# Kernel optimization log

Measured on AMD Instinct MI355X. Metric: run time of the kernel, lower is better.

## Reference

```python
import jax, jax.numpy as jnp
import numpy as np

NUM_HEADS = 16
SRC_FACTS = 4


def setup_inputs() -> dict:
    key = jax.random.key(0)
    k1, k2, k3, k4, k5 = jax.random.split(key, 5)
    B, S, H, Dh = 16, 512, NUM_HEADS, 64  # B = batch(4) * src_facts(4)
    D = H * Dh  # d_model = 1024
    pre_q = jax.random.normal(k1, (B, S, H, Dh), dtype=jnp.float32)
    pre_v = jax.random.normal(k2, (B, S, H, Dh), dtype=jnp.float32)
    pre_k = jax.random.normal(k3, (B, S, H, Dh), dtype=jnp.float32)
    attn_mask = jax.random.randint(k4, (B, S, S), 0, 2).astype(jnp.int32)
    output_weights = jax.random.normal(k5, (D, D), dtype=jnp.float32) / np.float32(np.sqrt(D))
    return {
        "pre_q": pre_q,
        "pre_v": pre_v,
        "pre_k": pre_k,
        "attn_mask": attn_mask,
        "output_weights": output_weights,
        "out_seq_len": 512,
        "d_model": 1024,
    }


def reference(pre_q, pre_v, pre_k, attn_mask, output_weights, out_seq_len, d_model):
    B, Sq, H, Dh = pre_q.shape
    # Original: K.sqrt(cast(d_model) // num_heads) -> sqrt(head_dim)
    scale = jnp.sqrt(jnp.float32(float(d_model) // H))
    mask = attn_mask.astype(jnp.float32)[:, None]  # (B, 1, q, k) broadcast over heads
    # scores: (B, H, q, k)
    scores = jnp.einsum("bqhd,bkhd->bhqk", pre_q, pre_k) / scale
    # multiplicative pre-mask + additive -1e9 on masked slots
    scores = scores * mask + (1.0 - mask) * jnp.float32(-1e9)
    # softmax then multiplicative post-mask
    attn = jax.nn.softmax(scores, axis=-1) * mask
    heads = jnp.einsum("bhqk,bkhd->bqhd", attn, pre_v)  # (B, q, H, Dh)
    out = heads.reshape(B, Sq, H * Dh) @ output_weights  # (B, q, d_model)
    return out.reshape(-1, SRC_FACTS, out_seq_len, d_model)
```

## Files before the change

kernel.cpp:

```cpp
#include <hip/hip_runtime.h>
#include <hip/hip_bf16.h>


typedef __bf16 bf16;
typedef bf16 bf16x8 __attribute__((ext_vector_type(8)));
typedef float floatx4 __attribute__((ext_vector_type(4)));
typedef unsigned short ushort8 __attribute__((ext_vector_type(8)));
typedef unsigned long long u64;

#define MFMA16(A, B, C) __builtin_amdgcn_mfma_f32_16x16x32_bf16((A), (B), (C), 0, 0, 0)

namespace {
constexpr int S   = 512;
constexpr int H   = 16;
constexpr int Dh  = 64;
constexpr int D   = 1024;
constexpr int LDT = 72;
constexpr size_t QN = (size_t)16 * S * H * Dh;
constexpr size_t WN = (size_t)D * D;
}

__global__ __launch_bounds__(256)
void prep_kernel(const float* __restrict__ Kf, const float* __restrict__ Vf,
                 const float* __restrict__ Wf, const int* __restrict__ Mg,
                 bf16* __restrict__ Kc, bf16* __restrict__ Vt,
                 bf16* __restrict__ Wt, u64* __restrict__ MB)
{
    __shared__ bf16 Ts[64 * LDT];
    const int blk = blockIdx.x, tid = threadIdx.x;

    if (blk < 4096) {
        const int i = blk * 256 + tid;
        const float* fs = Kf + (size_t)i * 8;
        bf16x8 v;
#pragma unroll
        for (int j = 0; j < 8; ++j) v[j] = (bf16)fs[j];
        *(bf16x8*)(Kc + (size_t)i * 8) = v;
    } else if (blk < 6144) {
        const int bk2 = blk - 4096;
        const int bh  = bk2 >> 3, st = bk2 & 7;
        const int b   = bh >> 4, h = bh & 15;
        const int r   = tid >> 2, c = (tid & 3) * 16;
        const float* src = Vf + ((size_t)((b * S + st * 64 + r) * H + h)) * Dh + c;
#pragma unroll
        for (int i = 0; i < 16; ++i)
            Ts[(c + i) * LDT + r] = (bf16)src[i];
        __syncthreads();
        bf16* dst = Vt + ((size_t)bh * 64 + r) * S + st * 64 + c;
        *(ushort8*)dst       = *(const ushort8*)&Ts[r * LDT + c];
        *(ushort8*)(dst + 8) = *(const ushort8*)&Ts[r * LDT + c + 8];
    } else if (blk < 6400) {
        const int bk2 = blk - 6144;
        const int nb  = bk2 & 15, kb = bk2 >> 4;
        const int r   = tid >> 2, c = (tid & 3) * 16;
        const float* src = Wf + (size_t)(kb * 64 + r) * D + nb * 64 + c;
#pragma unroll
        for (int i = 0; i < 16; ++i)
            Ts[(c + i) * LDT + r] = (bf16)src[i];
        __syncthreads();
        bf16* dst = Wt + (size_t)(nb * 64 + r) * D + kb * 64 + c;
        *(ushort8*)dst       = *(const ushort8*)&Ts[r * LDT + c];
        *(ushort8*)(dst + 8) = *(const ushort8*)&Ts[r * LDT + c + 8];
    } else {
        const int bk2  = blk - 6400;
        const int lane = tid & 63;
        const int idx4 = bk2 * 4 + (tid >> 6);
        const int row  = idx4 >> 1;
        const int half = idx4 & 1;
#pragma unroll
        for (int r = 0; r < 4; ++r) {
            int mv = Mg[(size_t)row * 512 + half * 256 + r * 64 + lane];
            u64 bm = __ballot(mv != 0);
            if (lane == 0) MB[(size_t)row * 8 + half * 4 + r] = bm;
        }
    }
}

__global__ __launch_bounds__(256)
void attn_kernel(const float* __restrict__ Qg, const bf16* __restrict__ Kc,
                 const bf16* __restrict__ Vtg, const u64* __restrict__ MB,
                 bf16* __restrict__ heads)
{
    __shared__ bf16 smem[(128 + 64 + 64) * LDT];
    bf16* Qs = smem;
    bf16* Ps = smem;
    bf16* Ks = smem + 128 * LDT;
    bf16* Vt = smem + 192 * LDT;

    const int tid  = threadIdx.x;
    const int lane = tid & 63;
    const int wave = tid >> 6;
    const int l15  = lane & 15;
    const int quad = lane >> 4;

    const int blk = blockIdx.x;
    const int h   = blk & 15;
    const int qt  = (blk >> 4) & 3;
    const int b   = blk >> 6;
    const int qbase = qt * 128;

    {
        const int pr = tid >> 1, pc = (tid & 1) * 32;
        const float* src = Qg + ((size_t)((b * S + qbase + pr) * H + h)) * Dh + pc;
#pragma unroll
        for (int ch = 0; ch < 4; ++ch) {
            bf16x8 v;
#pragma unroll
            for (int i = 0; i < 8; ++i) v[i] = (bf16)(src[ch * 8 + i] * 0.125f);
            *(bf16x8*)&Qs[pr * LDT + pc + ch * 8] = v;
        }
    }
    __syncthreads();
    bf16x8 aq[2][2];
#pragma unroll
    for (int mt = 0; mt < 2; ++mt)
#pragma unroll
        for (int hf = 0; hf < 2; ++hf)
            aq[mt][hf] = *(const bf16x8*)&Qs[(wave * 32 + mt * 16 + l15) * LDT + hf * 32 + quad * 8];

    float rsum[2][4] = {{0.f}};
    floatx4 O[2][4];
#pragma unroll
    for (int mt = 0; mt < 2; ++mt)
#pragma unroll
        for (int nt = 0; nt < 4; ++nt) O[mt][nt] = floatx4{0.f, 0.f, 0.f, 0.f};

    const int qw = qbase + wave * 32;
    const u64* mb_base = MB + ((size_t)b * S + qw) * 8;
    const bf16* vplane = Vtg + (size_t)(b * 16 + h) * 64 * S;

    const int sr = tid >> 2, sc_ = (tid & 3) * 16;

    for (int kt = 0; kt < 8; ++kt) {
        const int kb = kt * 64;
        const bf16* ksrc = Kc + ((size_t)((b * S + kb + sr) * H + h)) * Dh + sc_;
        const bf16* vsrc = vplane + (size_t)sr * S + kb + sc_;
        ushort8 k0 = *(const ushort8*)ksrc;
        ushort8 k1 = *(const ushort8*)(ksrc + 8);
        ushort8 v0 = *(const ushort8*)vsrc;
        ushort8 v1 = *(const ushort8*)(vsrc + 8);

        __syncthreads();
        *(ushort8*)&Ks[sr * LDT + sc_]     = k0;
        *(ushort8*)&Ks[sr * LDT + sc_ + 8] = k1;
        *(ushort8*)&Vt[sr * LDT + sc_]     = v0;
        *(ushort8*)&Vt[sr * LDT + sc_ + 8] = v1;
        __syncthreads();

        floatx4 sc4[2][4];
#pragma unroll
        for (int nt = 0; nt < 4; ++nt) {
            bf16x8 bk0 = *(const bf16x8*)&Ks[(nt * 16 + l15) * LDT + quad * 8];
            bf16x8 bk1 = *(const bf16x8*)&Ks[(nt * 16 + l15) * LDT + quad * 8 + 32];
#pragma unroll
            for (int mt = 0; mt < 2; ++mt) {
                floatx4 acc = floatx4{0.f, 0.f, 0.f, 0.f};
                acc = MFMA16(aq[mt][0], bk0, acc);
                acc = MFMA16(aq[mt][1], bk1, acc);
                sc4[mt][nt] = acc;
            }
        }

#pragma unroll
        for (int mt = 0; mt < 2; ++mt) {
#pragma unroll
            for (int reg = 0; reg < 4; ++reg) {
                const int row = mt * 16 + quad * 4 + reg;
                u64 m64 = mb_base[(size_t)row * 8 + kt];
                u64 t   = m64 >> l15;
#pragma unroll
                for (int nt = 0; nt < 4; ++nt) {
                    unsigned bit = (unsigned)(t >> (nt * 16)) & 1u;
                    float e = __expf(sc4[mt][nt][reg]);
                    float p = bit ? e : 0.f;
                    rsum[mt][reg] += p;
                    Ps[(wave * 32 + row) * LDT + nt * 16 + l15] = (bf16)p;
                }
            }
        }

#pragma unroll
        for (int nt = 0; nt < 4; ++nt) {
            bf16x8 bv0 = *(const bf16x8*)&Vt[(nt * 16 + l15) * LDT + quad * 8];
            bf16x8 bv1 = *(const bf16x8*)&Vt[(nt * 16 + l15) * LDT + quad * 8 + 32];
#pragma unroll
            for (int mt = 0; mt < 2; ++mt) {
                bf16x8 ap0 = *(const bf16x8*)&Ps[(wave * 32 + mt * 16 + l15) * LDT + quad * 8];
                bf16x8 ap1 = *(const bf16x8*)&Ps[(wave * 32 + mt * 16 + l15) * LDT + quad * 8 + 32];
                O[mt][nt] = MFMA16(ap0, bv0, O[mt][nt]);
                O[mt][nt] = MFMA16(ap1, bv1, O[mt][nt]);
            }
        }
    }

#pragma unroll
    for (int off = 1; off < 16; off <<= 1)
#pragma unroll
        for (int mt = 0; mt < 2; ++mt)
#pragma unroll
            for (int reg = 0; reg < 4; ++reg)
                rsum[mt][reg] += __shfl_xor(rsum[mt][reg], off, 64);

#pragma unroll
    for (int mt = 0; mt < 2; ++mt) {
        float inv[4];
#pragma unroll
        for (int reg = 0; reg < 4; ++reg)
            inv[reg] = (rsum[mt][reg] > 0.f) ? (1.f / rsum[mt][reg]) : 0.f;
#pragma unroll
        for (int nt = 0; nt < 4; ++nt) {
#pragma unroll
            for (int reg = 0; reg < 4; ++reg) {
                const int q = qw + mt * 16 + quad * 4 + reg;
                const int d = nt * 16 + l15;
                heads[((size_t)((b * S + q) * H + h)) * Dh + d] = (bf16)(O[mt][nt][reg] * inv[reg]);
            }
        }
    }
}

__global__ __launch_bounds__(256)
void proj_kernel(const bf16* __restrict__ A, const bf16* __restrict__ Wt,
                 float* __restrict__ out)
{
    __shared__ bf16 As[128 * LDT];
    __shared__ bf16 Ws[128 * LDT];

    const int tid  = threadIdx.x;
    const int lane = tid & 63;
    const int wave = tid >> 6;
    const int l15  = lane & 15;
    const int quad = lane >> 4;

    const int nb = blockIdx.x & 7;
    const int mb = blockIdx.x >> 3;
    const int mbase = mb * 128, nbase = nb * 128;
    const int wm = (wave & 1) * 64, wn = (wave >> 1) * 64;

    const int pr = tid >> 1, pc = (tid & 1) * 32;

    floatx4 O[4][4];
#pragma unroll
    for (int mt = 0; mt < 4; ++mt)
#pragma unroll
        for (int nt = 0; nt < 4; ++nt) O[mt][nt] = floatx4{0.f, 0.f, 0.f, 0.f};

    for (int kt = 0; kt < 16; ++kt) {
        const int kb = kt * 64;
        const bf16* asrc = A  + (size_t)(mbase + pr) * D + kb + pc;
        const bf16* wsrc = Wt + (size_t)(nbase + pr) * D + kb + pc;
        ushort8 a0 = *(const ushort8*)asrc;
        ushort8 a1 = *(const ushort8*)(asrc + 8);
        ushort8 a2 = *(const ushort8*)(asrc + 16);
        ushort8 a3 = *(const ushort8*)(asrc + 24);
        ushort8 w0 = *(const ushort8*)wsrc;
        ushort8 w1 = *(const ushort8*)(wsrc + 8);
        ushort8 w2 = *(const ushort8*)(wsrc + 16);
        ushort8 w3 = *(const ushort8*)(wsrc + 24);

        __syncthreads();
        *(ushort8*)&As[pr * LDT + pc]      = a0;
        *(ushort8*)&As[pr * LDT + pc + 8]  = a1;
        *(ushort8*)&As[pr * LDT + pc + 16] = a2;
        *(ushort8*)&As[pr * LDT + pc + 24] = a3;
        *(ushort8*)&Ws[pr * LDT + pc]      = w0;
        *(ushort8*)&Ws[pr * LDT + pc + 8]  = w1;
        *(ushort8*)&Ws[pr * LDT + pc + 16] = w2;
        *(ushort8*)&Ws[pr * LDT + pc + 24] = w3;
        __syncthreads();

        bf16x8 fa[4][2];
#pragma unroll
        for (int mt = 0; mt < 4; ++mt) {
            fa[mt][0] = *(const bf16x8*)&As[(wm + mt * 16 + l15) * LDT + quad * 8];
            fa[mt][1] = *(const bf16x8*)&As[(wm + mt * 16 + l15) * LDT + quad * 8 + 32];
        }
#pragma unroll
        for (int nt = 0; nt < 4; ++nt) {
            bf16x8 fb0 = *(const bf16x8*)&Ws[(wn + nt * 16 + l15) * LDT + quad * 8];
            bf16x8 fb1 = *(const bf16x8*)&Ws[(wn + nt * 16 + l15) * LDT + quad * 8 + 32];
#pragma unroll
            for (int mt = 0; mt < 4; ++mt) {
                O[mt][nt] = MFMA16(fa[mt][0], fb0, O[mt][nt]);
                O[mt][nt] = MFMA16(fa[mt][1], fb1, O[mt][nt]);
            }
        }
    }

#pragma unroll
    for (int mt = 0; mt < 4; ++mt) {
#pragma unroll
        for (int nt = 0; nt < 4; ++nt) {
#pragma unroll
            for (int reg = 0; reg < 4; ++reg) {
                const int m = mbase + wm + mt * 16 + quad * 4 + reg;
                const int n = nbase + wn + nt * 16 + l15;
                out[(size_t)m * D + n] = O[mt][nt][reg];
            }
        }
    }
}

extern "C" void kernel_launch(void* const* d_in, const int* in_sizes, int n_in,
                              void* d_out, int out_size, void* d_ws, size_t ws_size,
                              hipStream_t stream)
{
    const float* pre_q = (const float*)d_in[0];
    const float* pre_v = (const float*)d_in[1];
    const float* pre_k = (const float*)d_in[2];
    const int*   mask  = (const int*)d_in[3];
    const float* Wg    = (const float*)d_in[4];
    float* out = (float*)d_out;

    bf16* Kc    = (bf16*)d_ws;
    bf16* Vt    = Kc + QN;
    bf16* Wt    = Vt + QN;
    bf16* heads = Wt + WN;
    u64*  MB    = (u64*)(heads + QN);

    prep_kernel<<<10496, 256, 0, stream>>>(pre_k, pre_v, Wg, mask, Kc, Vt, Wt, MB);
    attn_kernel<<<1024, 256, 0, stream>>>(pre_q, Kc, Vt, MB, heads);
    proj_kernel<<<512, 256, 0, stream>>>(heads, Wt, out);
}
```

Measured before the change: 225.9 us.

## Compute transposed scores in registers to skip the P shared-memory round trip

The attention kernel now computes S^T = K·Q^T, with K rows loaded in a permuted order so that the MFMA output registers line up directly with the B-operand layout for the P·V MFMA. This removes the Q and P shared-memory staging and the per-element P stores and reloads. Each wave now handles 16 query rows instead of 32, so the grid doubles and launch bounds request 4 blocks per SM. The trade-off is that every K/V tile is loaded twice as often across blocks, and the mask word is read once per tile per row.

New measurement: 217.1 us. -3.9%, faster.

```diff
diff --git a/kernel.cpp b/kernel.cpp
--- a/kernel.cpp
+++ b/kernel.cpp
@@ -4,11 +4,12 @@
 
 typedef __bf16 bf16;
 typedef bf16 bf16x8 __attribute__((ext_vector_type(8)));
+typedef bf16 bf16x4 __attribute__((ext_vector_type(4)));
 typedef float floatx4 __attribute__((ext_vector_type(4)));
 typedef unsigned short ushort8 __attribute__((ext_vector_type(8)));
 typedef unsigned long long u64;
 
-#define MFMA16(A, B, C) __builtin_amdgcn_mfma_f32_16x16x32_bf16((A), (B), (C), 0, 0, 0)
+#define MFMA32(A, B, C) __builtin_amdgcn_mfma_f32_16x16x32_bf16((A), (B), (C), 0, 0, 0)
 
 namespace {
 constexpr int S   = 512;
@@ -76,16 +77,13 @@
     }
 }
 
-__global__ __launch_bounds__(256)
+__global__ __launch_bounds__(256, 4)
 void attn_kernel(const float* __restrict__ Qg, const bf16* __restrict__ Kc,
                  const bf16* __restrict__ Vtg, const u64* __restrict__ MB,
                  bf16* __restrict__ heads)
 {
-    __shared__ bf16 smem[(128 + 64 + 64) * LDT];
-    bf16* Qs = smem;
-    bf16* Ps = smem;
-    bf16* Ks = smem + 128 * LDT;
-    bf16* Vt = smem + 192 * LDT;
+    __shared__ bf16 Ks[64 * LDT];
+    __shared__ bf16 Vt[64 * LDT];
 
     const int tid  = threadIdx.x;
     const int lane = tid & 63;
@@ -95,50 +93,47 @@
 
     const int blk = blockIdx.x;
     const int h   = blk & 15;
-    const int qt  = (blk >> 4) & 3;
-    const int b   = blk >> 6;
-    const int qbase = qt * 128;
-
+    const int qt  = (blk >> 4) & 7;
+    const int b   = blk >> 7;
+    const int qw  = qt * 64 + wave * 16;
+
+    bf16x8 aq0, aq1;
     {
-        const int pr = tid >> 1, pc = (tid & 1) * 32;
-        const float* src = Qg + ((size_t)((b * S + qbase + pr) * H + h)) * Dh + pc;
-#pragma unroll
-        for (int ch = 0; ch < 4; ++ch) {
-            bf16x8 v;
-#pragma unroll
-            for (int i = 0; i < 8; ++i) v[i] = (bf16)(src[ch * 8 + i] * 0.125f);
-            *(bf16x8*)&Qs[pr * LDT + pc + ch * 8] = v;
-        }
-    }
-    __syncthreads();
-    bf16x8 aq[2][2];
-#pragma unroll
-    for (int mt = 0; mt < 2; ++mt)
-#pragma unroll
-        for (int hf = 0; hf < 2; ++hf)
-            aq[mt][hf] = *(const bf16x8*)&Qs[(wave * 32 + mt * 16 + l15) * LDT + hf * 32 + quad * 8];
-
-    float rsum[2][4] = {{0.f}};
-    floatx4 O[2][4];
-#pragma unroll
-    for (int mt = 0; mt < 2; ++mt)
-#pragma unroll
-        for (int nt = 0; nt < 4; ++nt) O[mt][nt] = floatx4{0.f, 0.f, 0.f, 0.f};
-
-    const int qw = qbase + wave * 32;
-    const u64* mb_base = MB + ((size_t)b * S + qw) * 8;
+        const float* qb = Qg + ((size_t)((b * S + qw + l15) * H + h)) * Dh + quad * 8;
+        floatx4 f0 = *(const floatx4*)qb;
+        floatx4 f1 = *(const floatx4*)(qb + 4);
+        floatx4 f2 = *(const floatx4*)(qb + 32);
+        floatx4 f3 = *(const floatx4*)(qb + 36);
+#pragma unroll
+        for (int j = 0; j < 4; ++j) {
+            aq0[j]     = (bf16)(f0[j] * 0.125f);
+            aq0[j + 4] = (bf16)(f1[j] * 0.125f);
+            aq1[j]     = (bf16)(f2[j] * 0.125f);
+            aq1[j + 4] = (bf16)(f3[j] * 0.125f);
+        }
+    }
+
+    float rsum = 0.f;
+    floatx4 O[4];
+#pragma unroll
+    for (int i = 0; i < 4; ++i) O[i] = floatx4{0.f, 0.f, 0.f, 0.f};
+
+    const u64* mbrow = MB + ((size_t)b * S + qw + l15) * 8;
     const bf16* vplane = Vtg + (size_t)(b * 16 + h) * 64 * S;
 
     const int sr = tid >> 2, sc_ = (tid & 3) * 16;
+    const int kperm = ((sr >> 5) << 5) | (((sr & 15) >> 2) << 3)
+                    | (((sr >> 4) & 1) << 2) | (sr & 3);
 
     for (int kt = 0; kt < 8; ++kt) {
         const int kb = kt * 64;
-        const bf16* ksrc = Kc + ((size_t)((b * S + kb + sr) * H + h)) * Dh + sc_;
+        const bf16* ksrc = Kc + ((size_t)((b * S + kb + kperm) * H + h)) * Dh + sc_;
         const bf16* vsrc = vplane + (size_t)sr * S + kb + sc_;
         ushort8 k0 = *(const ushort8*)ksrc;
         ushort8 k1 = *(const ushort8*)(ksrc + 8);
         ushort8 v0 = *(const ushort8*)vsrc;
         ushort8 v1 = *(const ushort8*)(vsrc + 8);
+        u64 m64 = mbrow[kt];
 
         __syncthreads();
         *(ushort8*)&Ks[sr * LDT + sc_]     = k0;
@@ -147,75 +142,47 @@
         *(ushort8*)&Vt[sr * LDT + sc_ + 8] = v1;
         __syncthreads();
 
-        floatx4 sc4[2][4];
-#pragma unroll
-        for (int nt = 0; nt < 4; ++nt) {
-            bf16x8 bk0 = *(const bf16x8*)&Ks[(nt * 16 + l15) * LDT + quad * 8];
-            bf16x8 bk1 = *(const bf16x8*)&Ks[(nt * 16 + l15) * LDT + quad * 8 + 32];
-#pragma unroll
-            for (int mt = 0; mt < 2; ++mt) {
-                floatx4 acc = floatx4{0.f, 0.f, 0.f, 0.f};
-                acc = MFMA16(aq[mt][0], bk0, acc);
-                acc = MFMA16(aq[mt][1], bk1, acc);
-                sc4[mt][nt] = acc;
-            }
-        }
-
-#pragma unroll
-        for (int mt = 0; mt < 2; ++mt) {
+        bf16x8 pB[2];
+#pragma unroll
+        for (int mt = 0; mt < 4; ++mt) {
+            bf16x8 ak0 = *(const bf16x8*)&Ks[(mt * 16 + l15) * LDT + quad * 8];
+            bf16x8 ak1 = *(const bf16x8*)&Ks[(mt * 16 + l15) * LDT + quad * 8 + 32];
+            floatx4 acc = floatx4{0.f, 0.f, 0.f, 0.f};
+            acc = MFMA32(ak0, aq0, acc);
+            acc = MFMA32(ak1, aq1, acc);
+            const int block = mt >> 1, tile = mt & 1;
+            const int kbase = block * 32 + quad * 8 + tile * 4;
 #pragma unroll
             for (int reg = 0; reg < 4; ++reg) {
-                const int row = mt * 16 + quad * 4 + reg;
-                u64 m64 = mb_base[(size_t)row * 8 + kt];
-                u64 t   = m64 >> l15;
-#pragma unroll
-                for (int nt = 0; nt < 4; ++nt) {
-                    unsigned bit = (unsigned)(t >> (nt * 16)) & 1u;
-                    float e = __expf(sc4[mt][nt][reg]);
-                    float p = bit ? e : 0.f;
-                    rsum[mt][reg] += p;
-                    Ps[(wave * 32 + row) * LDT + nt * 16 + l15] = (bf16)p;
-                }
-            }
-        }
-
-#pragma unroll
-        for (int nt = 0; nt < 4; ++nt) {
-            bf16x8 bv0 = *(const bf16x8*)&Vt[(nt * 16 + l15) * LDT + quad * 8];
-            bf16x8 bv1 = *(const bf16x8*)&Vt[(nt * 16 + l15) * LDT + quad * 8 + 32];
-#pragma unroll
-            for (int mt = 0; mt < 2; ++mt) {
-                bf16x8 ap0 = *(const bf16x8*)&Ps[(wave * 32 + mt * 16 + l15) * LDT + quad * 8];
-                bf16x8 ap1 = *(const bf16x8*)&Ps[(wave * 32 + mt * 16 + l15) * LDT + quad * 8 + 32];
-                O[mt][nt] = MFMA16(ap0, bv0, O[mt][nt]);
-                O[mt][nt] = MFMA16(ap1, bv1, O[mt][nt]);
-            }
-        }
-    }
-
-#pragma unroll
-    for (int off = 1; off < 16; off <<= 1)
-#pragma unroll
-        for (int mt = 0; mt < 2; ++mt)
-#pragma unroll
-            for (int reg = 0; reg < 4; ++reg)
-                rsum[mt][reg] += __shfl_xor(rsum[mt][reg], off, 64);
-
-#pragma unroll
-    for (int mt = 0; mt < 2; ++mt) {
-        float inv[4];
-#pragma unroll
-        for (int reg = 0; reg < 4; ++reg)
-            inv[reg] = (rsum[mt][reg] > 0.f) ? (1.f / rsum[mt][reg]) : 0.f;
-#pragma unroll
-        for (int nt = 0; nt < 4; ++nt) {
-#pragma unroll
-            for (int reg = 0; reg < 4; ++reg) {
-                const int q = qw + mt * 16 + quad * 4 + reg;
-                const int d = nt * 16 + l15;
-                heads[((size_t)((b * S + q) * H + h)) * Dh + d] = (bf16)(O[mt][nt][reg] * inv[reg]);
-            }
-        }
+                unsigned bit = (unsigned)(m64 >> (kbase + reg)) & 1u;
+                float e = __expf(acc[reg]);
+                float p = bit ? e : 0.f;
+                rsum += p;
+                pB[block][tile * 4 + reg] = (bf16)p;
+            }
+        }
+
+#pragma unroll
+        for (int block = 0; block < 2; ++block) {
+#pragma unroll
+            for (int mt = 0; mt < 4; ++mt) {
+                bf16x8 av = *(const bf16x8*)&Vt[(mt * 16 + l15) * LDT + block * 32 + quad * 8];
+                O[mt] = MFMA32(av, pB[block], O[mt]);
+            }
+        }
+    }
+
+    rsum += __shfl_xor(rsum, 16, 64);
+    rsum += __shfl_xor(rsum, 32, 64);
+    const float inv = (rsum > 0.f) ? (1.f / rsum) : 0.f;
+
+    bf16* hrow = heads + ((size_t)((b * S + qw + l15) * H + h)) * Dh;
+#pragma unroll
+    for (int mt = 0; mt < 4; ++mt) {
+        bf16x4 h4;
+#pragma unroll
+        for (int reg = 0; reg < 4; ++reg) h4[reg] = (bf16)(O[mt][reg] * inv);
+        *(bf16x4*)&hrow[mt * 16 + quad * 4] = h4;
     }
 }
 
@@ -281,8 +248,8 @@
             bf16x8 fb1 = *(const bf16x8*)&Ws[(wn + nt * 16 + l15) * LDT + quad * 8 + 32];
 #pragma unroll
             for (int mt = 0; mt < 4; ++mt) {
-                O[mt][nt] = MFMA16(fa[mt][0], fb0, O[mt][nt]);
-                O[mt][nt] = MFMA16(fa[mt][1], fb1, O[mt][nt]);
+                O[mt][nt] = MFMA32(fa[mt][0], fb0, O[mt][nt]);
+                O[mt][nt] = MFMA32(fa[mt][1], fb1, O[mt][nt]);
             }
         }
     }
@@ -319,6 +286,6 @@
     u64*  MB    = (u64*)(heads + QN);
 
     prep_kernel<<<10496, 256, 0, stream>>>(pre_k, pre_v, Wg, mask, Kc, Vt, Wt, MB);
-    attn_kernel<<<1024, 256, 0, stream>>>(pre_q, Kc, Vt, MB, heads);
+    attn_kernel<<<2048, 256, 0, stream>>>(pre_q, Kc, Vt, MB, heads);
     proj_kernel<<<512, 256, 0, stream>>>(heads, Wt, out);
 }
```
